# Kernel tuning notes

Measured on AMD Instinct MI355X. Metric: run time of the kernel, lower is better.

The kernel has to match this reference:

```python
import jax, jax.numpy as jnp
import numpy as np

SLOPE = 0.1  # supar MLP uses LeakyReLU(0.1)

def _mlp(x, W, b):
    return jax.nn.leaky_relu(x @ W + b, negative_slope=SLOPE)

def _triaffine(x, y, z, W):
    # supar Triaffine with n_out=1: s[b,z,x,y] = sum_{i,k,j} x[b,x,i] W[i,k,j] y[b,y,j] z[b,z,k]
    w = jnp.einsum('bzk,ikj->bzij', z, W)          # [b, n, d, d]
    return jnp.einsum('bxi,bzij,byj->bzxy', x, w, y)  # [b, n, n, n]

def _triu_sym(s):
    # s.triu() + s.triu(1).transpose(-1, -2) over last two dims
    return jnp.triu(s) + jnp.swapaxes(jnp.triu(s, 1), -1, -2)

def setup_inputs() -> dict:
    key = jax.random.key(0)
    B, N, D_IN, D = 2, 128, 1024, 150
    ks = jax.random.split(key, 16)
    sc_in = 1.0 / np.sqrt(D_IN)
    sc_tri = float(D) ** -1.5  # keeps triaffine outputs O(1)
    def nrm(k, shape, sc):
        return jax.random.normal(k, shape, jnp.float32) * sc
    return {
        'x':   jax.random.normal(ks[0], (B, N, D_IN), jnp.float32),
        'W_sh': nrm(ks[1], (D_IN, D), sc_in), 'b_sh': jnp.zeros((D,), jnp.float32),
        'W_st': nrm(ks[2], (D_IN, D), sc_in), 'b_st': jnp.zeros((D,), jnp.float32),
        'W_p':  nrm(ks[3], (D_IN, D), sc_in), 'b_p':  jnp.zeros((D,), jnp.float32),
        'T_pt':    nrm(ks[4], (D, D, D), sc_tri),
        'T_ph':    nrm(ks[5], (D, D, D), sc_tri),
        'T_phsib': nrm(ks[6], (D, D, D), sc_tri),
        'T_ptsib': nrm(ks[7], (D, D, D), sc_tri),
        'T_phcop': nrm(ks[8], (D, D, D), sc_tri),
        'T_ptcop': nrm(ks[9], (D, D, D), sc_tri),
    }

def reference(x, W_sh, b_sh, W_st, b_st, W_p, b_p,
              T_pt, T_ph, T_phsib, T_ptsib, T_phcop, T_ptcop):
    # eval mode: dropout is identity; ind_prd=False so p2 == p (shared MLP)
    sh = _mlp(x, W_sh, b_sh)
    st = _mlp(x, W_st, b_st)
    p = _mlp(x, W_p, b_p)
    p2 = p
    # span scores: [b, p, sh_idx, st_idx]
    span_pst = _triu_sym(_triaffine(sh, st, p2, T_pt))
    span_psh = _triaffine(sh, st, p, T_ph)
    # sibling scores: [b, p, h, h'] / [b, p, t, t']
    ph_sib = _triu_sym(_triaffine(sh, sh, p, T_phsib))
    pt_sib = _triu_sym(_triaffine(st, st, p2, T_ptsib))
    # co-parent scores: triaffine gives [b, h, p, p'], permute(0,2,3,1) -> [b, p, p', h]
    ph_cop = jnp.transpose(_triu_sym(_triaffine(p, p, sh, T_phcop)), (0, 2, 3, 1))
    pt_cop = jnp.transpose(_triu_sym(_triaffine(p2, p2, st, T_ptcop)), (0, 2, 3, 1))
    return (span_psh, span_pst, ph_sib, pt_sib, ph_cop, pt_cop)
```

## Files before the change

kernel.cpp:

```cpp
#include <hip/hip_runtime.h>


#define DD    150
#define KP    160
#define OUTBLK 4194304
#define NWZ   24064
#define TTG   3840000
#define WZG   (256*NWZ)
#define HROW  (256*160)

__device__ __forceinline__ unsigned short f2u(float f) {
  unsigned x = __float_as_uint(f);
  x += 0x7FFFu + ((x >> 16) & 1u);
  return (unsigned short)(x >> 16);
}

typedef __attribute__((ext_vector_type(8))) short frag8;
typedef __attribute__((ext_vector_type(4))) float facc4;

__constant__ int c_zsel[6] = {2, 2, 2, 2, 0, 1};
__constant__ int c_xsel[6] = {0, 0, 0, 1, 2, 2};
__constant__ int c_ysel[6] = {1, 1, 0, 1, 2, 2};

__global__ __launch_bounds__(256) void mlp_partial(
    const float* __restrict__ x,
    const float* __restrict__ W0, const float* __restrict__ W1, const float* __restrict__ W2,
    float* __restrict__ P)
{
  int m = blockIdx.x, bt = blockIdx.y, ks = blockIdx.z;
  const float* W = (m == 0) ? W0 : (m == 1) ? W1 : W2;
  int bn0 = bt * 32, k0 = ks * 128;
  __shared__ float xs[32][132];
  int tid = threadIdx.x;
  for (int e = 0; e < 4; ++e) {
    int l = e * 256 + tid;
    int row = l >> 5, c4 = l & 31;
    float4 v = *(const float4*)&x[(bn0 + row) * 1024 + k0 + c4 * 4];
    xs[row][c4 * 4 + 0] = v.x; xs[row][c4 * 4 + 1] = v.y;
    xs[row][c4 * 4 + 2] = v.z; xs[row][c4 * 4 + 3] = v.w;
  }
  __syncthreads();
  int tj = tid & 15, tt = tid >> 4, r = tt * 2;
  int dd[10];
  #pragma unroll
  for (int u = 0; u < 10; ++u) { int d = tj + 16 * u; dd[u] = d < 150 ? d : 149; }
  float a0[10], a1[10];
  #pragma unroll
  for (int u = 0; u < 10; ++u) { a0[u] = 0.f; a1[u] = 0.f; }
  for (int k = 0; k < 128; ++k) {
    float xa = xs[r][k], xb = xs[r + 1][k];
    const float* wr = W + (long long)(k0 + k) * 150;
    #pragma unroll
    for (int u = 0; u < 10; ++u) {
      float w = wr[dd[u]];
      a0[u] += xa * w; a1[u] += xb * w;
    }
  }
  float* Pb = P + (long long)(m * 8 + ks) * 256 * 160;
  #pragma unroll
  for (int u = 0; u < 10; ++u) {
    int d = tj + 16 * u;
    Pb[(bn0 + r) * 160 + d]     = a0[u];
    Pb[(bn0 + r + 1) * 160 + d] = a1[u];
  }
}

__global__ __launch_bounds__(256) void mlp_reduce(
    const float* __restrict__ P,
    const float* __restrict__ B0, const float* __restrict__ B1, const float* __restrict__ B2,
    unsigned short* __restrict__ H)
{
  int o = blockIdx.x * 256 + threadIdx.x;
  int d = o % 160;
  int bn = (o / 160) & 255;
  int m = o / (160 * 256);
  float v = 0.f;
  if (d < 150) {
    const float* Bv = (m == 0) ? B0 : (m == 1) ? B1 : B2;
    v = Bv[d];
    #pragma unroll
    for (int ks = 0; ks < 8; ++ks)
      v += P[((long long)(m * 8 + ks) * 256 + bn) * 160 + d];
    v = v > 0.f ? v : 0.1f * v;
  }
  H[o] = f2u(v);
}

struct TPtrs { const float* t[6]; };
__global__ __launch_bounds__(256) void tt_kernel(TPtrs tp, unsigned short* __restrict__ TT3)
{
  int i = blockIdx.x;
  int ky = blockIdx.y % 5, jy = blockIdx.y / 5;
  int k0 = ky * 32, j0 = jy * 32;
  int g = blockIdx.z;
  const float* T = tp.t[g];
  unsigned short* TT = TT3 + (long long)g * TTG;
  __shared__ float tl[32][33];
  int tid = threadIdx.x;
  #pragma unroll
  for (int e = 0; e < 4; ++e) {
    int l = e * 256 + tid;
    int r = l >> 5, c = l & 31;
    float v = 0.f;
    if (i < 150 && k0 + r < 150 && j0 + c < 150)
      v = T[i * 22500 + (k0 + r) * 150 + (j0 + c)];
    tl[r][c] = v;
  }
  __syncthreads();
  #pragma unroll
  for (int e = 0; e < 4; ++e) {
    int l = e * 256 + tid;
    int rr = l >> 5, cc = l & 31;
    if (j0 + rr < 150)
      TT[(long long)((j0 + rr) * 160 + i) * 160 + k0 + cc] = f2u(tl[cc][rr]);
  }
}

__global__ __launch_bounds__(256) void wz_gemm(
    const unsigned short* __restrict__ Hb, const unsigned short* __restrict__ TT3,
    unsigned short* __restrict__ wz3)
{
  constexpr int LR = 72;
  __shared__ unsigned short lA[128 * LR];
  __shared__ unsigned short lB[128 * LR];
  int g = blockIdx.z, tid = threadIdx.x;
  const unsigned short* Ab = Hb + c_zsel[g] * HROW + blockIdx.y * 128 * 160;
  const unsigned short* Bb = TT3 + (long long)g * TTG;
  int n0 = blockIdx.x * 128;
  int wave = tid >> 6, lane = tid & 63;
  int l15 = lane & 15, lq = lane >> 4;
  int mw = (wave & 1) * 64, nw = (wave >> 1) * 64;
  facc4 acc[4][4];
  #pragma unroll
  for (int i = 0; i < 4; ++i)
    #pragma unroll
    for (int j = 0; j < 4; ++j) acc[i][j] = (facc4){0.f, 0.f, 0.f, 0.f};
  for (int ch = 0; ch < 3; ++ch) {
    int k0 = ch << 6;
    int sh = (ch == 2) ? 2 : 3, upr = 1 << sh;
    for (int u = tid; u < 128 * upr; u += 256) {
      int row = u >> sh, off = (u & (upr - 1)) << 3;
      *(uint4*)&lA[row * LR + off] = *(const uint4*)&Ab[row * 160 + k0 + off];
    }
    for (int u = tid; u < 128 * upr; u += 256) {
      int row = u >> sh, off = (u & (upr - 1)) << 3;
      int gn = n0 + row;
      uint4 v; v.x = 0u; v.y = 0u; v.z = 0u; v.w = 0u;
      if (gn < 24000) v = *(const uint4*)&Bb[(long long)gn * 160 + k0 + off];
      *(uint4*)&lB[row * LR + off] = v;
    }
    __syncthreads();
    int nks = (ch == 2) ? 1 : 2;
    for (int ks = 0; ks < nks; ++ks) {
      int ko = (ks << 5) + (lq << 3);
      frag8 af[4], bfr[4];
      #pragma unroll
      for (int i = 0; i < 4; ++i) af[i] = *(const frag8*)&lA[(mw + i * 16 + l15) * LR + ko];
      #pragma unroll
      for (int j = 0; j < 4; ++j) bfr[j] = *(const frag8*)&lB[(nw + j * 16 + l15) * LR + ko];
      #pragma unroll
      for (int i = 0; i < 4; ++i)
        #pragma unroll
        for (int j = 0; j < 4; ++j)
          acc[i][j] = __builtin_amdgcn_mfma_f32_16x16x32_bf16(af[i], bfr[j], acc[i][j], 0, 0, 0);
    }
    __syncthreads();
  }
  unsigned short* C = wz3 + (long long)g * WZG;
  int mb = blockIdx.y * 128 + mw;
  #pragma unroll
  for (int i = 0; i < 4; ++i)
    #pragma unroll
    for (int r = 0; r < 4; ++r) {
      int m = mb + i * 16 + lq * 4 + r;
      #pragma unroll
      for (int j = 0; j < 4; ++j)
        C[(long long)m * NWZ + n0 + nw + j * 16 + l15] = f2u(acc[i][j][r]);
    }
}

struct SPtrs { float* p[6]; };
__global__ __launch_bounds__(256) void tmps_gemm(
    const unsigned short* __restrict__ Hb, const unsigned short* __restrict__ wz3,
    SPtrs sp)
{
  __shared__ union {
    struct { unsigned short A[128 * 72]; unsigned short B[160 * 72]; } p1;
    struct { unsigned short T[128 * 168]; unsigned short B[128 * 72]; } p2;
    float sq[128 * 128];
  } sm;

  int z = blockIdx.x, tid = threadIdx.x;
  int g = z >> 8, bz = z & 255, b = bz >> 7;
  const unsigned short* Ab = Hb + c_xsel[g] * HROW + b * 128 * 160;
  const unsigned short* Bb = wz3 + (long long)g * WZG + (long long)bz * NWZ;
  int wave = tid >> 6, lane = tid & 63;
  int l15 = lane & 15, lq = lane >> 4;
  int mw = (wave & 1) * 64;
  int nw80 = (wave >> 1) * 80, nw64 = (wave >> 1) * 64;

  facc4 acc[4][5];
  #pragma unroll
  for (int i = 0; i < 4; ++i)
    #pragma unroll
    for (int j = 0; j < 5; ++j) acc[i][j] = (facc4){0.f, 0.f, 0.f, 0.f};
  for (int ch = 0; ch < 3; ++ch) {
    int k0 = ch << 6;
    int sh = (ch == 2) ? 2 : 3, upr = 1 << sh;
    for (int u = tid; u < 128 * upr; u += 256) {
      int row = u >> sh, off = (u & (upr - 1)) << 3;
      *(uint4*)&sm.p1.A[row * 72 + off] = *(const uint4*)&Ab[row * 160 + k0 + off];
    }
    for (int u = tid; u < 160 * upr; u += 256) {
      int row = u >> sh, off = (u & (upr - 1)) << 3;
      uint4 v; v.x = 0u; v.y = 0u; v.z = 0u; v.w = 0u;
      if (row < 150) v = *(const uint4*)&Bb[row * 160 + k0 + off];
      *(uint4*)&sm.p1.B[row * 72 + off] = v;
    }
    __syncthreads();
    int nks = (ch == 2) ? 1 : 2;
    for (int ks = 0; ks < nks; ++ks) {
      int ko = (ks << 5) + (lq << 3);
      frag8 af[4], bfr[5];
      #pragma unroll
      for (int i = 0; i < 4; ++i) af[i] = *(const frag8*)&sm.p1.A[(mw + i * 16 + l15) * 72 + ko];
      #pragma unroll
      for (int j = 0; j < 5; ++j) bfr[j] = *(const frag8*)&sm.p1.B[(nw80 + j * 16 + l15) * 72 + ko];
      #pragma unroll
      for (int i = 0; i < 4; ++i)
        #pragma unroll
        for (int j = 0; j < 5; ++j)
          acc[i][j] = __builtin_amdgcn_mfma_f32_16x16x32_bf16(af[i], bfr[j], acc[i][j], 0, 0, 0);
    }
    __syncthreads();
  }

  #pragma unroll
  for (int i = 0; i < 4; ++i)
    #pragma unroll
    for (int r = 0; r < 4; ++r) {
      int m = mw + i * 16 + lq * 4 + r;
      #pragma unroll
      for (int j = 0; j < 5; ++j)
        sm.p2.T[m * 168 + nw80 + j * 16 + l15] = f2u(acc[i][j][r]);
    }

  const unsigned short* Yb = Hb + c_ysel[g] * HROW + b * 128 * 160;
  facc4 acc2[4][4];
  #pragma unroll
  for (int i = 0; i < 4; ++i)
    #pragma unroll
    for (int j = 0; j < 4; ++j) acc2[i][j] = (facc4){0.f, 0.f, 0.f, 0.f};
  for (int ch = 0; ch < 3; ++ch) {
    int k0 = ch << 6;
    int sh = (ch == 2) ? 2 : 3, upr = 1 << sh;
    __syncthreads();
    for (int u = tid; u < 128 * upr; u += 256) {
      int row = u >> sh, off = (u & (upr - 1)) << 3;
      *(uint4*)&sm.p2.B[row * 72 + off] = *(const uint4*)&Yb[row * 160 + k0 + off];
    }
    __syncthreads();
    int nks = (ch == 2) ? 1 : 2;
    for (int ks = 0; ks < nks; ++ks) {
      int ko = (ks << 5) + (lq << 3);
      frag8 af[4], bfr[4];
      #pragma unroll
      for (int i = 0; i < 4; ++i)
        af[i] = *(const frag8*)&sm.p2.T[(mw + i * 16 + l15) * 168 + k0 + ko];
      #pragma unroll
      for (int j = 0; j < 4; ++j)
        bfr[j] = *(const frag8*)&sm.p2.B[(nw64 + j * 16 + l15) * 72 + ko];
      #pragma unroll
      for (int i = 0; i < 4; ++i)
        #pragma unroll
        for (int j = 0; j < 4; ++j)
          acc2[i][j] = __builtin_amdgcn_mfma_f32_16x16x32_bf16(af[i], bfr[j], acc2[i][j], 0, 0, 0);
    }
  }

  float* C = sp.p[g] + (long long)bz * 16384;
  if (g >= 1 && g <= 3) {
    __syncthreads();
    #pragma unroll
    for (int i = 0; i < 4; ++i)
      #pragma unroll
      for (int r = 0; r < 4; ++r) {
        int m = mw + i * 16 + lq * 4 + r;
        #pragma unroll
        for (int j = 0; j < 4; ++j) {
          int n = nw64 + j * 16 + l15;
          sm.sq[m * 128 + (n ^ (m & 31))] = acc2[i][j][r];
        }
      }
    __syncthreads();
    #pragma unroll
    for (int i = 0; i < 4; ++i)
      #pragma unroll
      for (int r = 0; r < 4; ++r) {
        int m = mw + i * 16 + lq * 4 + r;
        #pragma unroll
        for (int j = 0; j < 4; ++j) {
          int n = nw64 + j * 16 + l15;
          int mn = m < n ? m : n;
          int mx = m ^ n ^ mn;
          C[m * 128 + n] = sm.sq[mn * 128 + (mx ^ (mn & 31))];
        }
      }
  } else if (g == 0) {
    #pragma unroll
    for (int i = 0; i < 4; ++i)
      #pragma unroll
      for (int r = 0; r < 4; ++r) {
        int m = mw + i * 16 + lq * 4 + r;
        #pragma unroll
        for (int j = 0; j < 4; ++j)
          C[m * 128 + nw64 + j * 16 + l15] = acc2[i][j][r];
      }
  } else {
    #pragma unroll
    for (int i = 0; i < 4; ++i)
      #pragma unroll
      for (int r = 0; r < 4; ++r) {
        int m = mw + i * 16 + lq * 4 + r;
        #pragma unroll
        for (int j = 0; j < 4; ++j) {
          int n = nw64 + j * 16 + l15;
          if (m <= n) C[m * 128 + n] = acc2[i][j][r];
        }
      }
  }
}

__global__ __launch_bounds__(256) void cop_kernel(
    const float* __restrict__ ss, float* __restrict__ out)
{
  int w0 = blockIdx.x << 5;
  int z0 = blockIdx.y << 5;
  int g  = blockIdx.z >> 1, b = blockIdx.z & 1;
  const float* sg = ss + (long long)g * OUTBLK;
  float* outp = out + (long long)(4 + g) * OUTBLK;
  __shared__ float tl[32][33];
  int tid = threadIdx.x;
  #pragma unroll
  for (int e = 0; e < 4; ++e) {
    int l = e * 256 + tid;
    int r = l >> 5, c = l & 31;
    int w = w0 + c;
    int xx = w >> 7, yy = w & 127;
    int sx = xx < yy ? xx : yy;
    int sy = xx < yy ? yy : xx;
    tl[r][c] = sg[(((b << 7) + z0 + r) << 14) + (sx << 7) + sy];
  }
  __syncthreads();
  #pragma unroll
  for (int e = 0; e < 4; ++e) {
    int l = e * 256 + tid;
    int rr = l >> 5, cc = l & 31;
    outp[(b << 21) + ((w0 + rr) << 7) + z0 + cc] = tl[cc][rr];
  }
}

extern "C" void kernel_launch(void* const* d_in, const int* in_sizes, int n_in,
                              void* d_out, int out_size, void* d_ws, size_t ws_size,
                              hipStream_t stream)
{
  const float* x   = (const float*)d_in[0];
  const float* Wsh = (const float*)d_in[1];
  const float* bsh = (const float*)d_in[2];
  const float* Wst = (const float*)d_in[3];
  const float* bst = (const float*)d_in[4];
  const float* Wp  = (const float*)d_in[5];
  const float* bp  = (const float*)d_in[6];
  TPtrs tp;
  tp.t[0] = (const float*)d_in[8];
  tp.t[1] = (const float*)d_in[7];
  tp.t[2] = (const float*)d_in[9];
  tp.t[3] = (const float*)d_in[10];
  tp.t[4] = (const float*)d_in[11];
  tp.t[5] = (const float*)d_in[12];
  float* out = (float*)d_out;
  char* wsb = (char*)d_ws;

  unsigned short* Hb   = (unsigned short*)(wsb);
  unsigned short* TT3  = (unsigned short*)(wsb + 245760);
  unsigned short* wz3  = (unsigned short*)(wsb + 46325760);
  float* P  = (float*)wz3;
  float* ss = (float*)TT3;

  SPtrs sp;
  sp.p[0] = out + 0LL * OUTBLK;
  sp.p[1] = out + 1LL * OUTBLK;
  sp.p[2] = out + 2LL * OUTBLK;
  sp.p[3] = out + 3LL * OUTBLK;
  sp.p[4] = ss;
  sp.p[5] = ss + OUTBLK;

  mlp_partial<<<dim3(3, 8, 8),    256, 0, stream>>>(x, Wsh, Wst, Wp, P);
  mlp_reduce <<<dim3(480),        256, 0, stream>>>(P, bsh, bst, bp, Hb);
  tt_kernel  <<<dim3(160, 25, 6), 256, 0, stream>>>(tp, TT3);
  wz_gemm    <<<dim3(188, 2, 6),  256, 0, stream>>>(Hb, TT3, wz3);
  tmps_gemm  <<<dim3(1536),       256, 0, stream>>>(Hb, wz3, sp);
  cop_kernel <<<dim3(512, 4, 4),  256, 0, stream>>>(ss, out);
}
```

Baseline: 368.3 us.

## Keep first triaffine GEMM result in registers via lane shuffles and restructure epilogue

The first GEMM in tmps_gemm is now computed transposed, one 32-row x strip per wave, so its accumulators can be packed to bf16 and rearranged with lane shuffles straight into A-operand fragments for the second GEMM. This removes the shared-memory write and read of the intermediate T tile and the chunked reloading of Y, which is now staged into LDS once. The symmetric epilogue is split into two 64-row halves with a padded shared buffer, which shrinks the LDS footprint, and launch bounds now request 3 blocks per SM. The cost is more register pressure from the accumulators and fragments, shuffle overhead, and extra barriers in the mirrored store path.

```diff
diff --git a/kernel.cpp b/kernel.cpp
--- a/kernel.cpp
+++ b/kernel.cpp
@@ -17,6 +17,7 @@
 
 typedef __attribute__((ext_vector_type(8))) short frag8;
 typedef __attribute__((ext_vector_type(4))) float facc4;
+typedef __attribute__((ext_vector_type(4))) unsigned uint4v;
 
 __constant__ int c_zsel[6] = {2, 2, 2, 2, 0, 1};
 __constant__ int c_xsel[6] = {0, 0, 0, 1, 2, 2};
@@ -180,154 +181,186 @@
 }
 
 struct SPtrs { float* p[6]; };
-__global__ __launch_bounds__(256) void tmps_gemm(
+__global__ __launch_bounds__(256, 3) void tmps_gemm(
     const unsigned short* __restrict__ Hb, const unsigned short* __restrict__ wz3,
     SPtrs sp)
 {
   __shared__ union {
-    struct { unsigned short A[128 * 72]; unsigned short B[160 * 72]; } p1;
-    struct { unsigned short T[128 * 168]; unsigned short B[128 * 72]; } p2;
-    float sq[128 * 128];
+    struct { unsigned short X[128 * 72]; unsigned short W[160 * 72]; } p1;
+    unsigned short Y[128 * 168];
+    float sq[64 * 129];
   } sm;
 
   int z = blockIdx.x, tid = threadIdx.x;
   int g = z >> 8, bz = z & 255, b = bz >> 7;
   const unsigned short* Ab = Hb + c_xsel[g] * HROW + b * 128 * 160;
-  const unsigned short* Bb = wz3 + (long long)g * WZG + (long long)bz * NWZ;
+  const unsigned short* Wb = wz3 + (long long)g * WZG + (long long)bz * NWZ;
   int wave = tid >> 6, lane = tid & 63;
   int l15 = lane & 15, lq = lane >> 4;
-  int mw = (wave & 1) * 64;
-  int nw80 = (wave >> 1) * 80, nw64 = (wave >> 1) * 64;
-
-  facc4 acc[4][5];
-  #pragma unroll
-  for (int i = 0; i < 4; ++i)
-    #pragma unroll
-    for (int j = 0; j < 5; ++j) acc[i][j] = (facc4){0.f, 0.f, 0.f, 0.f};
+  int X0 = wave * 32;
+
+  facc4 accT[10][2];
+  #pragma unroll
+  for (int jt = 0; jt < 10; ++jt)
+    #pragma unroll
+    for (int xt = 0; xt < 2; ++xt) accT[jt][xt] = (facc4){0.f, 0.f, 0.f, 0.f};
   for (int ch = 0; ch < 3; ++ch) {
     int k0 = ch << 6;
     int sh = (ch == 2) ? 2 : 3, upr = 1 << sh;
     for (int u = tid; u < 128 * upr; u += 256) {
       int row = u >> sh, off = (u & (upr - 1)) << 3;
-      *(uint4*)&sm.p1.A[row * 72 + off] = *(const uint4*)&Ab[row * 160 + k0 + off];
+      *(uint4*)&sm.p1.X[row * 72 + off] = *(const uint4*)&Ab[row * 160 + k0 + off];
     }
     for (int u = tid; u < 160 * upr; u += 256) {
       int row = u >> sh, off = (u & (upr - 1)) << 3;
       uint4 v; v.x = 0u; v.y = 0u; v.z = 0u; v.w = 0u;
-      if (row < 150) v = *(const uint4*)&Bb[row * 160 + k0 + off];
-      *(uint4*)&sm.p1.B[row * 72 + off] = v;
+      if (row < 150) v = *(const uint4*)&Wb[row * 160 + k0 + off];
+      *(uint4*)&sm.p1.W[row * 72 + off] = v;
     }
     __syncthreads();
     int nks = (ch == 2) ? 1 : 2;
     for (int ks = 0; ks < nks; ++ks) {
       int ko = (ks << 5) + (lq << 3);
-      frag8 af[4], bfr[5];
-      #pragma unroll
-      for (int i = 0; i < 4; ++i) af[i] = *(const frag8*)&sm.p1.A[(mw + i * 16 + l15) * 72 + ko];
-      #pragma unroll
-      for (int j = 0; j < 5; ++j) bfr[j] = *(const frag8*)&sm.p1.B[(nw80 + j * 16 + l15) * 72 + ko];
-      #pragma unroll
-      for (int i = 0; i < 4; ++i)
-        #pragma unroll
-        for (int j = 0; j < 5; ++j)
-          acc[i][j] = __builtin_amdgcn_mfma_f32_16x16x32_bf16(af[i], bfr[j], acc[i][j], 0, 0, 0);
-    }
-    __syncthreads();
-  }
-
-  #pragma unroll
-  for (int i = 0; i < 4; ++i)
-    #pragma unroll
-    for (int r = 0; r < 4; ++r) {
-      int m = mw + i * 16 + lq * 4 + r;
-      #pragma unroll
-      for (int j = 0; j < 5; ++j)
-        sm.p2.T[m * 168 + nw80 + j * 16 + l15] = f2u(acc[i][j][r]);
-    }
+      frag8 bx0 = *(const frag8*)&sm.p1.X[(X0 + l15) * 72 + ko];
+      frag8 bx1 = *(const frag8*)&sm.p1.X[(X0 + 16 + l15) * 72 + ko];
+      #pragma unroll
+      for (int jt = 0; jt < 10; ++jt) {
+        frag8 aw = *(const frag8*)&sm.p1.W[(jt * 16 + l15) * 72 + ko];
+        accT[jt][0] = __builtin_amdgcn_mfma_f32_16x16x32_bf16(aw, bx0, accT[jt][0], 0, 0, 0);
+        accT[jt][1] = __builtin_amdgcn_mfma_f32_16x16x32_bf16(aw, bx1, accT[jt][1], 0, 0, 0);
+      }
+    }
+    __syncthreads();
+  }
+
+  frag8 pA[2][5];
+  {
+    int s0 = ((lq & 1) << 5) + l15;
+    int s2 = s0 + 16;
+    bool lo = lq < 2;
+    #pragma unroll
+    for (int kb = 0; kb < 5; ++kb)
+      #pragma unroll
+      for (int xt = 0; xt < 2; ++xt) {
+        unsigned w0l = (unsigned)f2u(accT[2 * kb][xt][0]) |
+                       ((unsigned)f2u(accT[2 * kb][xt][1]) << 16);
+        unsigned w1l = (unsigned)f2u(accT[2 * kb][xt][2]) |
+                       ((unsigned)f2u(accT[2 * kb][xt][3]) << 16);
+        unsigned w0h = (unsigned)f2u(accT[2 * kb + 1][xt][0]) |
+                       ((unsigned)f2u(accT[2 * kb + 1][xt][1]) << 16);
+        unsigned w1h = (unsigned)f2u(accT[2 * kb + 1][xt][2]) |
+                       ((unsigned)f2u(accT[2 * kb + 1][xt][3]) << 16);
+        unsigned a0 = __shfl(w0l, s0), b0 = __shfl(w0h, s0);
+        unsigned a1 = __shfl(w1l, s0), b1 = __shfl(w1h, s0);
+        unsigned a2 = __shfl(w0l, s2), b2 = __shfl(w0h, s2);
+        unsigned a3 = __shfl(w1l, s2), b3 = __shfl(w1h, s2);
+        uint4v uv;
+        uv.x = lo ? a0 : b0;
+        uv.y = lo ? a1 : b1;
+        uv.z = lo ? a2 : b2;
+        uv.w = lo ? a3 : b3;
+        pA[xt][kb] = __builtin_bit_cast(frag8, uv);
+      }
+  }
 
   const unsigned short* Yb = Hb + c_ysel[g] * HROW + b * 128 * 160;
-  facc4 acc2[4][4];
-  #pragma unroll
-  for (int i = 0; i < 4; ++i)
-    #pragma unroll
-    for (int j = 0; j < 4; ++j) acc2[i][j] = (facc4){0.f, 0.f, 0.f, 0.f};
-  for (int ch = 0; ch < 3; ++ch) {
-    int k0 = ch << 6;
-    int sh = (ch == 2) ? 2 : 3, upr = 1 << sh;
-    __syncthreads();
-    for (int u = tid; u < 128 * upr; u += 256) {
-      int row = u >> sh, off = (u & (upr - 1)) << 3;
-      *(uint4*)&sm.p2.B[row * 72 + off] = *(const uint4*)&Yb[row * 160 + k0 + off];
-    }
-    __syncthreads();
-    int nks = (ch == 2) ? 1 : 2;
-    for (int ks = 0; ks < nks; ++ks) {
-      int ko = (ks << 5) + (lq << 3);
-      frag8 af[4], bfr[4];
-      #pragma unroll
-      for (int i = 0; i < 4; ++i)
-        af[i] = *(const frag8*)&sm.p2.T[(mw + i * 16 + l15) * 168 + k0 + ko];
-      #pragma unroll
-      for (int j = 0; j < 4; ++j)
-        bfr[j] = *(const frag8*)&sm.p2.B[(nw64 + j * 16 + l15) * 72 + ko];
-      #pragma unroll
-      for (int i = 0; i < 4; ++i)
-        #pragma unroll
-        for (int j = 0; j < 4; ++j)
-          acc2[i][j] = __builtin_amdgcn_mfma_f32_16x16x32_bf16(af[i], bfr[j], acc2[i][j], 0, 0, 0);
+  {
+    int y = tid & 127, part = tid >> 7;
+    #pragma unroll
+    for (int p = 0; p < 10; ++p) {
+      int off = part * 80 + p * 8;
+      *(uint4*)&sm.Y[y * 168 + off] = *(const uint4*)&Yb[y * 160 + off];
+    }
+  }
+  __syncthreads();
+
+  facc4 acc2[2][8];
+  #pragma unroll
+  for (int xt = 0; xt < 2; ++xt)
+    #pragma unroll
+    for (int yt = 0; yt < 8; ++yt) acc2[xt][yt] = (facc4){0.f, 0.f, 0.f, 0.f};
+  #pragma unroll
+  for (int ks = 0; ks < 5; ++ks) {
+    int ko = (ks << 5) + (lq << 3);
+    #pragma unroll
+    for (int yt = 0; yt < 8; ++yt) {
+      frag8 by = *(const frag8*)&sm.Y[(yt * 16 + l15) * 168 + ko];
+      acc2[0][yt] = __builtin_amdgcn_mfma_f32_16x16x32_bf16(pA[0][ks], by, acc2[0][yt], 0, 0, 0);
+      acc2[1][yt] = __builtin_amdgcn_mfma_f32_16x16x32_bf16(pA[1][ks], by, acc2[1][yt], 0, 0, 0);
     }
   }
 
   float* C = sp.p[g] + (long long)bz * 16384;
-  if (g >= 1 && g <= 3) {
-    __syncthreads();
-    #pragma unroll
-    for (int i = 0; i < 4; ++i)
+  if (g == 0) {
+    #pragma unroll
+    for (int xt = 0; xt < 2; ++xt)
       #pragma unroll
       for (int r = 0; r < 4; ++r) {
-        int m = mw + i * 16 + lq * 4 + r;
-        #pragma unroll
-        for (int j = 0; j < 4; ++j) {
-          int n = nw64 + j * 16 + l15;
-          sm.sq[m * 128 + (n ^ (m & 31))] = acc2[i][j][r];
+        int x = X0 + xt * 16 + lq * 4 + r;
+        #pragma unroll
+        for (int yt = 0; yt < 8; ++yt)
+          C[x * 128 + yt * 16 + l15] = acc2[xt][yt][r];
+      }
+  } else if (g >= 4) {
+    #pragma unroll
+    for (int xt = 0; xt < 2; ++xt)
+      #pragma unroll
+      for (int r = 0; r < 4; ++r) {
+        int x = X0 + xt * 16 + lq * 4 + r;
+        #pragma unroll
+        for (int yt = 0; yt < 8; ++yt) {
+          int y = yt * 16 + l15;
+          if (x <= y) C[x * 128 + y] = acc2[xt][yt][r];
         }
       }
-    __syncthreads();
-    #pragma unroll
-    for (int i = 0; i < 4; ++i)
+  } else {
+    #pragma unroll
+    for (int xt = 0; xt < 2; ++xt)
       #pragma unroll
       for (int r = 0; r < 4; ++r) {
-        int m = mw + i * 16 + lq * 4 + r;
-        #pragma unroll
-        for (int j = 0; j < 4; ++j) {
-          int n = nw64 + j * 16 + l15;
-          int mn = m < n ? m : n;
-          int mx = m ^ n ^ mn;
-          C[m * 128 + n] = sm.sq[mn * 128 + (mx ^ (mn & 31))];
+        int x = X0 + xt * 16 + lq * 4 + r;
+        #pragma unroll
+        for (int yt = 0; yt < 8; ++yt) {
+          int y = yt * 16 + l15;
+          if (y >= x) C[x * 128 + y] = acc2[xt][yt][r];
         }
       }
-  } else if (g == 0) {
-    #pragma unroll
-    for (int i = 0; i < 4; ++i)
-      #pragma unroll
-      for (int r = 0; r < 4; ++r) {
-        int m = mw + i * 16 + lq * 4 + r;
-        #pragma unroll
-        for (int j = 0; j < 4; ++j)
-          C[m * 128 + nw64 + j * 16 + l15] = acc2[i][j][r];
-      }
-  } else {
-    #pragma unroll
-    for (int i = 0; i < 4; ++i)
-      #pragma unroll
-      for (int r = 0; r < 4; ++r) {
-        int m = mw + i * 16 + lq * 4 + r;
-        #pragma unroll
-        for (int j = 0; j < 4; ++j) {
-          int n = nw64 + j * 16 + l15;
-          if (m <= n) C[m * 128 + n] = acc2[i][j][r];
+    __syncthreads();
+    if (wave < 2) {
+      #pragma unroll
+      for (int xt = 0; xt < 2; ++xt)
+        #pragma unroll
+        for (int r = 0; r < 4; ++r) {
+          int x = X0 + xt * 16 + lq * 4 + r;
+          #pragma unroll
+          for (int yt = 0; yt < 8; ++yt)
+            sm.sq[x * 129 + yt * 16 + l15] = acc2[xt][yt][r];
         }
-      }
+    }
+    __syncthreads();
+    for (int it = 0; it < 32; ++it) {
+      int x = X0 + it;
+      int y = lane;
+      if (y < 64 && y < x) C[x * 128 + y] = sm.sq[y * 129 + x];
+    }
+    __syncthreads();
+    if (wave >= 2) {
+      #pragma unroll
+      for (int xt = 0; xt < 2; ++xt)
+        #pragma unroll
+        for (int r = 0; r < 4; ++r) {
+          int x = X0 + xt * 16 + lq * 4 + r;
+          #pragma unroll
+          for (int yt = 0; yt < 8; ++yt)
+            sm.sq[(x - 64) * 129 + yt * 16 + l15] = acc2[xt][yt][r];
+        }
+    }
+    __syncthreads();
+    for (int it = 0; it < 16; ++it) {
+      int x = 64 + wave * 16 + it;
+      int y = 64 + lane;
+      if (y < x) C[x * 128 + y] = sm.sq[(y - 64) * 129 + x];
+    }
   }
 }
 
```

Result: no change. 370.1 us (+0.5%).
